# Performance work log

Measured on AMD Instinct MI355X. Metric: run time of the kernel, lower is better.

The kernel has to match this reference:

```python
import jax, jax.numpy as jnp
import numpy as np

LN_EPS = 1e-5
DEN_EPS = 1e-5


def _layernorm(x, gamma, beta):
    mu = jnp.mean(x, axis=-1, keepdims=True)
    var = jnp.mean((x - mu) ** 2, axis=-1, keepdims=True)
    return (x - mu) * jax.lax.rsqrt(var + LN_EPS) * gamma + beta


def setup_inputs() -> dict:
    key = jax.random.key(0)
    ks = jax.random.split(key, 10)
    B, T, Fin, D = 4, 1024, 256, 128
    s = 0.02
    return {
        "x": jax.random.normal(ks[0], (B, T, Fin), jnp.float32),
        "S0": jnp.zeros((B, 1, D, D), jnp.float32),
        "Z0": jnp.zeros((B, 1, D), jnp.float32),
        "ln_gamma": jnp.ones((Fin,), jnp.float32),
        "ln_beta": jnp.zeros((Fin,), jnp.float32),
        "Wk": jax.random.normal(ks[1], (D, Fin), jnp.float32) * s,
        "Wq": jax.random.normal(ks[2], (D, Fin), jnp.float32) * s,
        "Wv": jax.random.normal(ks[3], (D, Fin), jnp.float32) * s,
        "W1": jax.random.normal(ks[4], (D, D), jnp.float32) * s,
        "b1": jnp.zeros((D,), jnp.float32),
        "W2": jax.random.normal(ks[5], (D, D), jnp.float32) * s,
        "b2": jnp.zeros((D,), jnp.float32),
        "Ws": jax.random.normal(ks[6], (D, Fin), jnp.float32) * s,
        "bs": jnp.zeros((D,), jnp.float32),
    }


def reference(x, S0, Z0, ln_gamma, ln_beta, Wk, Wq, Wv, W1, b1, W2, b2, Ws, bs):
    xn = _layernorm(x, ln_gamma, ln_beta)            # [B,T,Fin]
    phi = lambda z: jax.nn.elu(z) + 1.0
    K = phi(jnp.einsum('btf,df->btd', xn, Wk))       # [B,T,D]
    Q = phi(jnp.einsum('btf,df->btd', xn, Wq))
    V = jnp.einsum('btf,df->btd', xn, Wv)
    # running-sum aggregation of K outer V, seeded by carried state
    KV = jnp.einsum('bti,btj->btij', K, V)           # [B,T,D,D]
    S = jnp.cumsum(KV, axis=1) + S0                  # [B,T,D,D]
    Z = jnp.cumsum(K, axis=1) + Z0                   # [B,T,D]
    num = jnp.einsum('bti,btil->btl', Q, S)          # [B,T,D]
    den = jnp.einsum('btl,btl->bt', Q, Z)[..., None] + DEN_EPS
    out = num / den
    out = jax.nn.relu(jnp.einsum('btd,ed->bte', out, W1) + b1)
    out = jax.nn.relu(jnp.einsum('btd,ed->bte', out, W2) + b2)
    out = out + jnp.einsum('btf,df->btd', xn, Ws) + bs
    return (out, S, Z)
```

## Files before the change

kernel.cpp:

```cpp
#include <hip/hip_runtime.h>
#include <math.h>

#define BB 4
#define TT 1024
#define FIN 256
#define DD 128
#define CL 16
#define NC 64
#define ROWS (BB*TT)

__global__ __launch_bounds__(256) void k_ln_qkv(
    const float* __restrict__ x, const float* __restrict__ gamma, const float* __restrict__ beta,
    const float* __restrict__ Wk, const float* __restrict__ Wq, const float* __restrict__ Wv,
    const float* __restrict__ Ws, const float* __restrict__ bs,
    float* __restrict__ Kp, float* __restrict__ Qp, float* __restrict__ Vp, float* __restrict__ XSp)
{
    __shared__ float xt[8][FIN];
    const int tid  = threadIdx.x;
    const int row0 = blockIdx.x * 8;

    {
        const int r = tid >> 5, l = tid & 31;
        const float* xr = x + (size_t)(row0 + r) * FIN + l * 8;
        float v[8];
        #pragma unroll
        for (int k = 0; k < 8; ++k) v[k] = xr[k];
        float s = 0.f, sq = 0.f;
        #pragma unroll
        for (int k = 0; k < 8; ++k) { s += v[k]; sq += v[k] * v[k]; }
        #pragma unroll
        for (int m = 16; m >= 1; m >>= 1) {
            s  += __shfl_xor(s,  m, 64);
            sq += __shfl_xor(sq, m, 64);
        }
        const float mu  = s * (1.0f / FIN);
        const float var = sq * (1.0f / FIN) - mu * mu;
        const float rs  = rsqrtf(var + 1e-5f);
        #pragma unroll
        for (int k = 0; k < 8; ++k) {
            const int f = l * 8 + k;
            xt[r][f] = (v[k] - mu) * rs * gamma[f] + beta[f];
        }
    }
    __syncthreads();

    const int m0 = tid >> 7;
    const int d  = tid & 127;
    const int m1 = (tid + 256) >> 7;
    const float* W0 = (m0 == 0 ? Wk : Wq) + (size_t)d * FIN;
    const float* W1r = (m1 == 2 ? Wv : Ws) + (size_t)d * FIN;

    float acc0[8], acc1[8];
    #pragma unroll
    for (int r = 0; r < 8; ++r) { acc0[r] = 0.f; acc1[r] = 0.f; }

    for (int k4 = 0; k4 < FIN / 4; ++k4) {
        const float4 w0 = ((const float4*)W0)[k4];
        const float4 w1 = ((const float4*)W1r)[k4];
        #pragma unroll
        for (int r = 0; r < 8; ++r) {
            const float4 xv = ((const float4*)xt[r])[k4];
            acc0[r] += w0.x * xv.x + w0.y * xv.y + w0.z * xv.z + w0.w * xv.w;
            acc1[r] += w1.x * xv.x + w1.y * xv.y + w1.z * xv.z + w1.w * xv.w;
        }
    }

    float* dst0 = (m0 == 0 ? Kp : Qp);
    float* dst1 = (m1 == 2 ? Vp : XSp);
    const float bsv = (m1 == 3) ? bs[d] : 0.f;
    #pragma unroll
    for (int r = 0; r < 8; ++r) {
        float a = acc0[r];
        a = (a > 0.f) ? (a + 1.f) : expf(a);
        dst0[(size_t)(row0 + r) * DD + d] = a;
        dst1[(size_t)(row0 + r) * DD + d] = acc1[r] + bsv;
    }
}

__global__ __launch_bounds__(256) void k_chunksum(
    const float* __restrict__ Kp, const float* __restrict__ Vp,
    float* __restrict__ SKV, float* __restrict__ SK)
{
    __shared__ float Kb[CL][DD];
    __shared__ float Vb[CL][DD];
    const int tid = threadIdx.x;
    const int c = blockIdx.x & (NC - 1);
    const int b = blockIdx.x >> 6;
    const size_t base = (size_t)(b * TT + c * CL) * DD;

    #pragma unroll
    for (int q = 0; q < 2; ++q) {
        const int fi = q * 256 + tid;
        ((float4*)&Kb[0][0])[fi] = ((const float4*)(Kp + base))[fi];
        ((float4*)&Vb[0][0])[fi] = ((const float4*)(Vp + base))[fi];
    }
    __syncthreads();

    const int j = tid & 127, hi = tid >> 7;
    float acc[64];
    #pragma unroll
    for (int w = 0; w < 64; ++w) acc[w] = 0.f;

    for (int t = 0; t < CL; ++t) {
        const float vj = Vb[t][j];
        #pragma unroll
        for (int w4 = 0; w4 < 16; ++w4) {
            const float4 kf = *(const float4*)&Kb[t][hi * 64 + w4 * 4];
            acc[w4 * 4 + 0] += kf.x * vj;
            acc[w4 * 4 + 1] += kf.y * vj;
            acc[w4 * 4 + 2] += kf.z * vj;
            acc[w4 * 4 + 3] += kf.w * vj;
        }
    }

    float* out = SKV + (size_t)(b * NC + c) * DD * DD;
    #pragma unroll
    for (int w = 0; w < 64; ++w) {
        const int i = hi * 64 + w;
        out[(size_t)i * DD + j] = acc[w];
    }
    if (tid < DD) {
        float s = 0.f;
        #pragma unroll
        for (int t = 0; t < CL; ++t) s += Kb[t][tid];
        SK[(size_t)(b * NC + c) * DD + tid] = s;
    }
}

__global__ __launch_bounds__(256) void k_prefix(
    const float* __restrict__ SKV, const float* __restrict__ SK,
    const float* __restrict__ S0, const float* __restrict__ Z0,
    float* __restrict__ Sout, float* __restrict__ Zout)
{
    const int gid = blockIdx.x * 256 + threadIdx.x;
    const int b = gid >> 14, e = gid & 16383;
    float acc = S0[(size_t)b * 16384 + e];
    const float* p = SKV + (size_t)b * NC * 16384 + e;
    float* so = Sout + (size_t)b * TT * 16384 + (size_t)(CL - 1) * 16384 + e;
    for (int c = 0; c < NC; ++c) {
        acc += p[(size_t)c * 16384];
        so[(size_t)c * CL * 16384] = acc;
    }
    if (gid < BB * DD) {
        const int b2 = gid >> 7, i = gid & 127;
        float z = Z0[b2 * DD + i];
        for (int c = 0; c < NC; ++c) {
            z += SK[(size_t)(b2 * NC + c) * DD + i];
            Zout[(size_t)(b2 * TT + c * CL + CL - 1) * DD + i] = z;
        }
    }
}

__global__ __launch_bounds__(256) void k_scan(
    const float* __restrict__ Kp, const float* __restrict__ Qp, const float* __restrict__ Vp,
    const float* __restrict__ S0, const float* __restrict__ Z0,
    float* __restrict__ Sout, float* __restrict__ Zout, float* __restrict__ NUM)
{
    __shared__ float Kb[CL][DD];
    __shared__ float Qb[CL][DD];
    __shared__ float Vb[CL][64];
    __shared__ float4 nred[2][4][16];

    const int tid  = threadIdx.x;
    const int half = blockIdx.x & 1;
    const int c    = (blockIdx.x >> 1) & (NC - 1);
    const int b    = blockIdx.x >> 7;
    const int j0   = half * 64;
    const size_t rbase = (size_t)(b * TT + c * CL);

    {
        const float4* Ksrc = (const float4*)(Kp + rbase * DD);
        const float4* Qsrc = (const float4*)(Qp + rbase * DD);
        #pragma unroll
        for (int q = 0; q < 2; ++q) {
            const int fi = q * 256 + tid;
            ((float4*)&Kb[0][0])[fi] = Ksrc[fi];
            ((float4*)&Qb[0][0])[fi] = Qsrc[fi];
        }
        const int tv = tid >> 4, gv = tid & 15;
        ((float4*)&Vb[0][0])[tid] = *(const float4*)(Vp + (rbase + tv) * DD + j0 + gv * 4);
    }

    const int g = tid & 15, h = tid >> 4;
    float4 acc[8];
    {
        const float* src = (c == 0) ? (S0 + (size_t)b * 16384)
                                    : (Sout + ((size_t)(b * TT) + c * CL - 1) * 16384);
        #pragma unroll
        for (int w = 0; w < 8; ++w) {
            const int i = w * 16 + h;
            acc[w] = *(const float4*)(src + (size_t)i * DD + j0 + g * 4);
        }
    }
    float zacc = 0.f;
    const bool doZ = (half == 0) && (tid < DD);
    if (doZ) {
        zacc = (c == 0) ? Z0[b * DD + tid]
                        : Zout[((size_t)(b * TT) + c * CL - 1) * DD + tid];
    }
    __syncthreads();

    const int wav = tid >> 6;
    for (int t = 0; t < CL; ++t) {
        const size_t tt = rbase + t;
        const float4 v4 = *(const float4*)&Vb[t][g * 4];
        float4 np; np.x = np.y = np.z = np.w = 0.f;
        float* srow = Sout + tt * 16384 + j0 + g * 4;
        #pragma unroll
        for (int w = 0; w < 8; ++w) {
            const int i = w * 16 + h;
            const float kk = Kb[t][i];
            const float qq = Qb[t][i];
            acc[w].x += kk * v4.x; acc[w].y += kk * v4.y;
            acc[w].z += kk * v4.z; acc[w].w += kk * v4.w;
            if (t < CL - 1) *(float4*)(srow + (size_t)i * DD) = acc[w];
            np.x += qq * acc[w].x; np.y += qq * acc[w].y;
            np.z += qq * acc[w].z; np.w += qq * acc[w].w;
        }
        #pragma unroll
        for (int m = 16; m <= 32; m <<= 1) {
            np.x += __shfl_xor(np.x, m, 64);
            np.y += __shfl_xor(np.y, m, 64);
            np.z += __shfl_xor(np.z, m, 64);
            np.w += __shfl_xor(np.w, m, 64);
        }
        if ((tid & 63) < 16) nred[t & 1][wav][g] = np;
        if (doZ) {
            zacc += Kb[t][tid];
            if (t < CL - 1) Zout[tt * DD + tid] = zacc;
        }
        __syncthreads();
        if (tid < 16) {
            const float4 r0 = nred[t & 1][0][tid], r1 = nred[t & 1][1][tid];
            const float4 r2 = nred[t & 1][2][tid], r3 = nred[t & 1][3][tid];
            float4 o;
            o.x = r0.x + r1.x + r2.x + r3.x;
            o.y = r0.y + r1.y + r2.y + r3.y;
            o.z = r0.z + r1.z + r2.z + r3.z;
            o.w = r0.w + r1.w + r2.w + r3.w;
            *(float4*)(NUM + tt * DD + j0 + tid * 4) = o;
        }
    }
}

__global__ __launch_bounds__(256) void k_mlp(
    const float* __restrict__ NUM, const float* __restrict__ Qp,
    const float* __restrict__ Zp, const float* __restrict__ XSp,
    const float* __restrict__ W1, const float* __restrict__ b1,
    const float* __restrict__ W2, const float* __restrict__ b2,
    float* __restrict__ Oout)
{
    __shared__ float h0[16][DD];
    __shared__ float h1[16][DD];
    __shared__ float parr[16][256];
    __shared__ float denl[16];
    const int tid = threadIdx.x;
    const int d = tid & 127, s = tid >> 7;
    const int row0 = blockIdx.x * 16;

    float4 w1r[16], w2r[16];
    #pragma unroll
    for (int k4 = 0; k4 < 16; ++k4) {
        w1r[k4] = *(const float4*)(W1 + (size_t)d * DD + s * 64 + k4 * 4);
        w2r[k4] = *(const float4*)(W2 + (size_t)d * DD + s * 64 + k4 * 4);
    }

    {
        const int r = tid >> 4, kk = tid & 15;
        const float* qrow = Qp + (size_t)(row0 + r) * DD + kk * 8;
        const float* zrow = Zp + (size_t)(row0 + r) * DD + kk * 8;
        float sden = 0.f;
        #pragma unroll
        for (int u = 0; u < 8; ++u) sden += qrow[u] * zrow[u];
        #pragma unroll
        for (int m = 1; m <= 8; m <<= 1) sden += __shfl_xor(sden, m, 64);
        if (kk == 0) denl[r] = sden + 1e-5f;
    }
    __syncthreads();

    #pragma unroll
    for (int q = 0; q < 8; ++q) {
        const int f = q * 256 + tid;
        const int r = f >> 7, dd2 = f & 127;
        h0[r][dd2] = NUM[(size_t)row0 * DD + f] / denl[r];
    }
    __syncthreads();

    #pragma unroll
    for (int r = 0; r < 16; ++r) {
        float pp = 0.f;
        #pragma unroll
        for (int k4 = 0; k4 < 16; ++k4) {
            const float4 xv = *(const float4*)&h0[r][s * 64 + k4 * 4];
            pp += w1r[k4].x * xv.x + w1r[k4].y * xv.y + w1r[k4].z * xv.z + w1r[k4].w * xv.w;
        }
        parr[r][tid] = pp;
    }
    __syncthreads();
    #pragma unroll
    for (int q = 0; q < 8; ++q) {
        const int f = q * 256 + tid;
        const int r = f >> 7, dd2 = f & 127;
        h1[r][dd2] = fmaxf(parr[r][dd2] + parr[r][dd2 + 128] + b1[dd2], 0.f);
    }
    __syncthreads();

    #pragma unroll
    for (int r = 0; r < 16; ++r) {
        float pp = 0.f;
        #pragma unroll
        for (int k4 = 0; k4 < 16; ++k4) {
            const float4 xv = *(const float4*)&h1[r][s * 64 + k4 * 4];
            pp += w2r[k4].x * xv.x + w2r[k4].y * xv.y + w2r[k4].z * xv.z + w2r[k4].w * xv.w;
        }
        parr[r][tid] = pp;
    }
    __syncthreads();
    #pragma unroll
    for (int q = 0; q < 8; ++q) {
        const int f = q * 256 + tid;
        const int r = f >> 7, dd2 = f & 127;
        const float hv = fmaxf(parr[r][dd2] + parr[r][dd2 + 128] + b2[dd2], 0.f);
        Oout[(size_t)row0 * DD + f] = hv + XSp[(size_t)row0 * DD + f];
    }
}

extern "C" void kernel_launch(void* const* d_in, const int* in_sizes, int n_in,
                              void* d_out, int out_size, void* d_ws, size_t ws_size,
                              hipStream_t stream)
{
    const float* x  = (const float*)d_in[0];
    const float* S0 = (const float*)d_in[1];
    const float* Z0 = (const float*)d_in[2];
    const float* g  = (const float*)d_in[3];
    const float* be = (const float*)d_in[4];
    const float* Wk = (const float*)d_in[5];
    const float* Wq = (const float*)d_in[6];
    const float* Wv = (const float*)d_in[7];
    const float* W1 = (const float*)d_in[8];
    const float* b1 = (const float*)d_in[9];
    const float* W2 = (const float*)d_in[10];
    const float* b2 = (const float*)d_in[11];
    const float* Ws = (const float*)d_in[12];
    const float* bs = (const float*)d_in[13];

    float* outp = (float*)d_out;
    float* Sout = outp + (size_t)ROWS * DD;
    float* Zout = Sout + (size_t)BB * TT * DD * DD;

    float* ws  = (float*)d_ws;
    float* Kp  = ws;
    float* Qp  = Kp + (size_t)ROWS * DD;
    float* Vp  = Qp + (size_t)ROWS * DD;
    float* XSp = Vp + (size_t)ROWS * DD;
    float* NUM = XSp + (size_t)ROWS * DD;
    float* SKV = NUM + (size_t)ROWS * DD;
    float* SK  = SKV + (size_t)BB * NC * DD * DD;

    k_ln_qkv  <<<ROWS / 8, 256, 0, stream>>>(x, g, be, Wk, Wq, Wv, Ws, bs, Kp, Qp, Vp, XSp);
    k_chunksum<<<BB * NC, 256, 0, stream>>>(Kp, Vp, SKV, SK);
    k_prefix  <<<BB * DD * DD / 256, 256, 0, stream>>>(SKV, SK, S0, Z0, Sout, Zout);
    k_scan    <<<BB * NC * 2, 256, 0, stream>>>(Kp, Qp, Vp, S0, Z0, Sout, Zout, NUM);
    k_mlp     <<<ROWS / 16, 256, 0, stream>>>(NUM, Qp, Zout, XSp, W1, b1, W2, b2, outp);
}
```

Measured before the change: 381.3 us.

## Compute numerator via chunked linear attention and fuse with MLP; slim scan kernel

Replaces per-timestep numerator accumulation in the scan with a chunked formulation: Q times the chunk-start state plus an intra-chunk causal QK^T matrix times V, fused into the MLP kernel along with the denominator and Z outputs. The scan kernel now only writes S, with blocks split over the i dimension so each wave writes wider contiguous rows and no longer needs cross-wave reductions or per-step barriers. The prefix kernel batches its strided loads eight at a time to expose memory parallelism. The fused kernel reads chunk-end states from Sout written by the prefix kernel, so it depends on launch ordering, and it uses much more shared memory, which may lower occupancy.

```diff
diff --git a/kernel.cpp b/kernel.cpp
--- a/kernel.cpp
+++ b/kernel.cpp
@@ -137,126 +137,53 @@
     float acc = S0[(size_t)b * 16384 + e];
     const float* p = SKV + (size_t)b * NC * 16384 + e;
     float* so = Sout + (size_t)b * TT * 16384 + (size_t)(CL - 1) * 16384 + e;
-    for (int c = 0; c < NC; ++c) {
-        acc += p[(size_t)c * 16384];
-        so[(size_t)c * CL * 16384] = acc;
+    for (int c0 = 0; c0 < NC; c0 += 8) {
+        float v[8];
+        #pragma unroll
+        for (int q = 0; q < 8; ++q) v[q] = p[(size_t)(c0 + q) * 16384];
+        #pragma unroll
+        for (int q = 0; q < 8; ++q) { acc += v[q]; so[(size_t)(c0 + q) * CL * 16384] = acc; }
     }
     if (gid < BB * DD) {
         const int b2 = gid >> 7, i = gid & 127;
         float z = Z0[b2 * DD + i];
-        for (int c = 0; c < NC; ++c) {
-            z += SK[(size_t)(b2 * NC + c) * DD + i];
-            Zout[(size_t)(b2 * TT + c * CL + CL - 1) * DD + i] = z;
-        }
-    }
-}
-
-__global__ __launch_bounds__(256) void k_scan(
-    const float* __restrict__ Kp, const float* __restrict__ Qp, const float* __restrict__ Vp,
-    const float* __restrict__ S0, const float* __restrict__ Z0,
-    float* __restrict__ Sout, float* __restrict__ Zout, float* __restrict__ NUM)
-{
-    __shared__ float Kb[CL][DD];
-    __shared__ float Qb[CL][DD];
-    __shared__ float Vb[CL][64];
-    __shared__ float4 nred[2][4][16];
-
-    const int tid  = threadIdx.x;
-    const int half = blockIdx.x & 1;
-    const int c    = (blockIdx.x >> 1) & (NC - 1);
-    const int b    = blockIdx.x >> 7;
-    const int j0   = half * 64;
-    const size_t rbase = (size_t)(b * TT + c * CL);
-
-    {
-        const float4* Ksrc = (const float4*)(Kp + rbase * DD);
-        const float4* Qsrc = (const float4*)(Qp + rbase * DD);
-        #pragma unroll
-        for (int q = 0; q < 2; ++q) {
-            const int fi = q * 256 + tid;
-            ((float4*)&Kb[0][0])[fi] = Ksrc[fi];
-            ((float4*)&Qb[0][0])[fi] = Qsrc[fi];
-        }
-        const int tv = tid >> 4, gv = tid & 15;
-        ((float4*)&Vb[0][0])[tid] = *(const float4*)(Vp + (rbase + tv) * DD + j0 + gv * 4);
-    }
-
-    const int g = tid & 15, h = tid >> 4;
-    float4 acc[8];
-    {
-        const float* src = (c == 0) ? (S0 + (size_t)b * 16384)
-                                    : (Sout + ((size_t)(b * TT) + c * CL - 1) * 16384);
-        #pragma unroll
-        for (int w = 0; w < 8; ++w) {
-            const int i = w * 16 + h;
-            acc[w] = *(const float4*)(src + (size_t)i * DD + j0 + g * 4);
-        }
-    }
-    float zacc = 0.f;
-    const bool doZ = (half == 0) && (tid < DD);
-    if (doZ) {
-        zacc = (c == 0) ? Z0[b * DD + tid]
-                        : Zout[((size_t)(b * TT) + c * CL - 1) * DD + tid];
-    }
-    __syncthreads();
-
-    const int wav = tid >> 6;
-    for (int t = 0; t < CL; ++t) {
-        const size_t tt = rbase + t;
-        const float4 v4 = *(const float4*)&Vb[t][g * 4];
-        float4 np; np.x = np.y = np.z = np.w = 0.f;
-        float* srow = Sout + tt * 16384 + j0 + g * 4;
-        #pragma unroll
-        for (int w = 0; w < 8; ++w) {
-            const int i = w * 16 + h;
-            const float kk = Kb[t][i];
-            const float qq = Qb[t][i];
-            acc[w].x += kk * v4.x; acc[w].y += kk * v4.y;
-            acc[w].z += kk * v4.z; acc[w].w += kk * v4.w;
-            if (t < CL - 1) *(float4*)(srow + (size_t)i * DD) = acc[w];
-            np.x += qq * acc[w].x; np.y += qq * acc[w].y;
-            np.z += qq * acc[w].z; np.w += qq * acc[w].w;
-        }
-        #pragma unroll
-        for (int m = 16; m <= 32; m <<= 1) {
-            np.x += __shfl_xor(np.x, m, 64);
-            np.y += __shfl_xor(np.y, m, 64);
-            np.z += __shfl_xor(np.z, m, 64);
-            np.w += __shfl_xor(np.w, m, 64);
-        }
-        if ((tid & 63) < 16) nred[t & 1][wav][g] = np;
-        if (doZ) {
-            zacc += Kb[t][tid];
-            if (t < CL - 1) Zout[tt * DD + tid] = zacc;
-        }
-        __syncthreads();
-        if (tid < 16) {
-            const float4 r0 = nred[t & 1][0][tid], r1 = nred[t & 1][1][tid];
-            const float4 r2 = nred[t & 1][2][tid], r3 = nred[t & 1][3][tid];
-            float4 o;
-            o.x = r0.x + r1.x + r2.x + r3.x;
-            o.y = r0.y + r1.y + r2.y + r3.y;
-            o.z = r0.z + r1.z + r2.z + r3.z;
-            o.w = r0.w + r1.w + r2.w + r3.w;
-            *(float4*)(NUM + tt * DD + j0 + tid * 4) = o;
-        }
-    }
-}
-
-__global__ __launch_bounds__(256) void k_mlp(
-    const float* __restrict__ NUM, const float* __restrict__ Qp,
-    const float* __restrict__ Zp, const float* __restrict__ XSp,
+        const float* pk = SK + (size_t)b2 * NC * DD + i;
+        float* zo = Zout + ((size_t)b2 * TT + CL - 1) * DD + i;
+        for (int c0 = 0; c0 < NC; c0 += 8) {
+            float v[8];
+            #pragma unroll
+            for (int q = 0; q < 8; ++q) v[q] = pk[(size_t)(c0 + q) * DD];
+            #pragma unroll
+            for (int q = 0; q < 8; ++q) { z += v[q]; zo[(size_t)(c0 + q) * CL * DD] = z; }
+        }
+    }
+}
+
+__global__ __launch_bounds__(256) void k_num_mlp(
+    const float* __restrict__ Qp, const float* __restrict__ Kp, const float* __restrict__ Vp,
+    const float* __restrict__ XSp, const float* __restrict__ S0, const float* __restrict__ Z0,
     const float* __restrict__ W1, const float* __restrict__ b1,
     const float* __restrict__ W2, const float* __restrict__ b2,
+    const float* Sce,
+    float* Zout,
     float* __restrict__ Oout)
 {
-    __shared__ float h0[16][DD];
-    __shared__ float h1[16][DD];
-    __shared__ float parr[16][256];
-    __shared__ float denl[16];
+    __shared__ float Qb[CL][132];
+    __shared__ float Kb[CL][132];
+    __shared__ float Vb[CL][DD];
+    __shared__ float Ab[CL][CL];
+    __shared__ float zs[DD];
+    __shared__ float red[2][CL][DD];
+    __shared__ float h0[CL][DD];
+    __shared__ float h1[CL][DD];
+    __shared__ float parr[CL][256];
+    __shared__ float denl[CL];
+
     const int tid = threadIdx.x;
+    const int c = blockIdx.x & (NC - 1);
+    const int b = blockIdx.x >> 6;
+    const size_t rbase = (size_t)(b * TT + c * CL);
     const int d = tid & 127, s = tid >> 7;
-    const int row0 = blockIdx.x * 16;
 
     float4 w1r[16], w2r[16];
     #pragma unroll
@@ -265,24 +192,78 @@
         w2r[k4] = *(const float4*)(W2 + (size_t)d * DD + s * 64 + k4 * 4);
     }
 
-    {
-        const int r = tid >> 4, kk = tid & 15;
-        const float* qrow = Qp + (size_t)(row0 + r) * DD + kk * 8;
-        const float* zrow = Zp + (size_t)(row0 + r) * DD + kk * 8;
-        float sden = 0.f;
-        #pragma unroll
-        for (int u = 0; u < 8; ++u) sden += qrow[u] * zrow[u];
-        #pragma unroll
-        for (int m = 1; m <= 8; m <<= 1) sden += __shfl_xor(sden, m, 64);
-        if (kk == 0) denl[r] = sden + 1e-5f;
-    }
-    __syncthreads();
-
-    #pragma unroll
-    for (int q = 0; q < 8; ++q) {
-        const int f = q * 256 + tid;
-        const int r = f >> 7, dd2 = f & 127;
-        h0[r][dd2] = NUM[(size_t)row0 * DD + f] / denl[r];
+    #pragma unroll
+    for (int q = 0; q < 2; ++q) {
+        const int idx = q * 256 + tid;
+        const int t = idx >> 5, jq = idx & 31;
+        *(float4*)&Qb[t][jq * 4] = *(const float4*)(Qp + (rbase + t) * DD + jq * 4);
+        *(float4*)&Kb[t][jq * 4] = *(const float4*)(Kp + (rbase + t) * DD + jq * 4);
+        ((float4*)&Vb[0][0])[idx] = ((const float4*)(Vp + rbase * DD))[idx];
+    }
+    if (tid < DD)
+        zs[tid] = (c == 0) ? Z0[b * DD + tid] : Zout[(rbase - 1) * DD + tid];
+    __syncthreads();
+
+    {
+        const int t = tid >> 4, u = tid & 15;
+        float a = 0.f;
+        #pragma unroll
+        for (int k4 = 0; k4 < 32; ++k4) {
+            const float4 q4 = *(const float4*)&Qb[t][k4 * 4];
+            const float4 kv = *(const float4*)&Kb[u][k4 * 4];
+            a += q4.x * kv.x + q4.y * kv.y + q4.z * kv.z + q4.w * kv.w;
+        }
+        const float am = (u <= t) ? a : 0.f;
+        Ab[t][u] = am;
+        float dz = 0.f;
+        #pragma unroll
+        for (int kk = 0; kk < 8; ++kk) dz += Qb[t][u * 8 + kk] * zs[u * 8 + kk];
+        float r = am + dz;
+        #pragma unroll
+        for (int m = 1; m <= 8; m <<= 1) r += __shfl_xor(r, m, 64);
+        if (u == 0) denl[t] = r + 1e-5f;
+    }
+
+    if (tid < DD) {
+        float z = zs[tid];
+        for (int t = 0; t < CL - 1; ++t) {
+            z += Kb[t][tid];
+            Zout[(rbase + t) * DD + tid] = z;
+        }
+    }
+    __syncthreads();
+
+    {
+        float nt[CL];
+        #pragma unroll
+        for (int t = 0; t < CL; ++t) nt[t] = 0.f;
+        const float* sst = (c == 0) ? (S0 + (size_t)b * 16384)
+                                    : (Sce + (rbase - 1) * 16384);
+        #pragma unroll 4
+        for (int k4 = s * 16; k4 < s * 16 + 16; ++k4) {
+            const int k = k4 * 4;
+            const float sv0 = sst[(size_t)(k + 0) * DD + d];
+            const float sv1 = sst[(size_t)(k + 1) * DD + d];
+            const float sv2 = sst[(size_t)(k + 2) * DD + d];
+            const float sv3 = sst[(size_t)(k + 3) * DD + d];
+            #pragma unroll
+            for (int t = 0; t < CL; ++t) {
+                const float4 q4 = *(const float4*)&Qb[t][k];
+                nt[t] += q4.x * sv0 + q4.y * sv1 + q4.z * sv2 + q4.w * sv3;
+            }
+        }
+        #pragma unroll
+        for (int t = 0; t < CL; ++t) red[s][t][d] = nt[t];
+    }
+    __syncthreads();
+
+    #pragma unroll
+    for (int tl = 0; tl < 8; ++tl) {
+        const int t = s * 8 + tl;
+        float num = red[0][t][d] + red[1][t][d];
+        #pragma unroll
+        for (int u = 0; u < CL; ++u) num += Ab[t][u] * Vb[u][d];
+        h0[t][d] = num / denl[t];
     }
     __syncthreads();
 
@@ -321,7 +302,52 @@
         const int f = q * 256 + tid;
         const int r = f >> 7, dd2 = f & 127;
         const float hv = fmaxf(parr[r][dd2] + parr[r][dd2 + 128] + b2[dd2], 0.f);
-        Oout[(size_t)row0 * DD + f] = hv + XSp[(size_t)row0 * DD + f];
+        Oout[rbase * DD + f] = hv + XSp[rbase * DD + f];
+    }
+}
+
+__global__ __launch_bounds__(256) void k_scan(
+    const float* __restrict__ Kp, const float* __restrict__ Vp,
+    const float* __restrict__ S0, float* Sout)
+{
+    __shared__ float Kb[CL][64];
+    __shared__ float Vb[CL][DD];
+    const int tid = threadIdx.x;
+    const int ih  = blockIdx.x & 1;
+    const int c   = (blockIdx.x >> 1) & (NC - 1);
+    const int b   = blockIdx.x >> 7;
+    const int i0  = ih * 64;
+    const size_t rbase = (size_t)(b * TT + c * CL);
+
+    {
+        const float4* Vsrc = (const float4*)(Vp + rbase * DD);
+        ((float4*)&Vb[0][0])[tid]       = Vsrc[tid];
+        ((float4*)&Vb[0][0])[256 + tid] = Vsrc[256 + tid];
+        const int tv = tid >> 4, gk = tid & 15;
+        *(float4*)&Kb[tv][gk * 4] = *(const float4*)(Kp + (rbase + tv) * DD + i0 + gk * 4);
+    }
+
+    const int g = tid & 31, h = tid >> 5;
+    float4 acc[8];
+    {
+        const float* src = (c == 0) ? (S0 + (size_t)b * 16384)
+                                    : (Sout + ((size_t)(b * TT) + c * CL - 1) * 16384);
+        #pragma unroll
+        for (int w = 0; w < 8; ++w)
+            acc[w] = *(const float4*)(src + (size_t)(i0 + w * 8 + h) * DD + g * 4);
+    }
+    __syncthreads();
+
+    float* sbase = Sout + rbase * 16384 + (size_t)i0 * DD + g * 4;
+    for (int t = 0; t < CL - 1; ++t) {
+        const float4 v4 = *(const float4*)&Vb[t][g * 4];
+        #pragma unroll
+        for (int w = 0; w < 8; ++w) {
+            const float kk = Kb[t][w * 8 + h];
+            acc[w].x += kk * v4.x; acc[w].y += kk * v4.y;
+            acc[w].z += kk * v4.z; acc[w].w += kk * v4.w;
+            *(float4*)(sbase + (size_t)t * 16384 + (size_t)(w * 8 + h) * DD) = acc[w];
+        }
     }
 }
 
@@ -353,13 +379,13 @@
     float* Qp  = Kp + (size_t)ROWS * DD;
     float* Vp  = Qp + (size_t)ROWS * DD;
     float* XSp = Vp + (size_t)ROWS * DD;
-    float* NUM = XSp + (size_t)ROWS * DD;
-    float* SKV = NUM + (size_t)ROWS * DD;
+    float* SKV = XSp + (size_t)ROWS * DD;
     float* SK  = SKV + (size_t)BB * NC * DD * DD;
 
     k_ln_qkv  <<<ROWS / 8, 256, 0, stream>>>(x, g, be, Wk, Wq, Wv, Ws, bs, Kp, Qp, Vp, XSp);
     k_chunksum<<<BB * NC, 256, 0, stream>>>(Kp, Vp, SKV, SK);
     k_prefix  <<<BB * DD * DD / 256, 256, 0, stream>>>(SKV, SK, S0, Z0, Sout, Zout);
-    k_scan    <<<BB * NC * 2, 256, 0, stream>>>(Kp, Qp, Vp, S0, Z0, Sout, Zout, NUM);
-    k_mlp     <<<ROWS / 16, 256, 0, stream>>>(NUM, Qp, Zout, XSp, W1, b1, W2, b2, outp);
-}
+    k_num_mlp <<<BB * NC, 256, 0, stream>>>(Qp, Kp, Vp, XSp, S0, Z0,
+                                            W1, b1, W2, b2, Sout, Zout, outp);
+    k_scan    <<<BB * NC * 2, 256, 0, stream>>>(Kp, Vp, S0, Sout);
+}
```

After: 391.0 us. 2.5% more time.
